# Optimization experiments

Measured on AMD Instinct MI355X. Metric: run time of the kernel, lower is better.

## Reference

```python
import jax, jax.numpy as jnp
import numpy as np

B, T, IN, H, S, OUT, NB = 64, 2048, 32, 256, 256, 32, 4
EPS = 1e-5


def setup_inputs() -> dict:
    key = jax.random.key(0)
    ks = jax.random.split(key, 13)

    def w(k, shape, fan_in):
        lim = 1.0 / np.sqrt(fan_in)
        return jax.random.uniform(k, shape, minval=-lim, maxval=lim, dtype=jnp.float32)

    return {
        "x": jax.random.normal(ks[0], (B, T, IN), dtype=jnp.float32),
        "enc_w": w(ks[1], (H, IN), IN),
        "enc_b": w(ks[2], (H,), IN),
        "wih": w(ks[3], (NB, 3 * S, H), H),    # GRU input weights per block
        "whh": w(ks[4], (NB, 3 * S, S), S),    # GRU hidden weights per block
        "b_ih": w(ks[5], (NB, 3 * S), S),      # GRU bias
        "b_n": w(ks[6], (NB, S), S),           # GRU candidate bias (bias_n)
        "g1w": w(ks[7], (NB, H, S), S),        # GLU value proj
        "g1b": w(ks[8], (NB, H), S),
        "g2w": w(ks[9], (NB, H, S), S),        # GLU gate proj
        "g2b": w(ks[10], (NB, H), S),
        "dec_w": w(ks[11], (OUT, H), H),
        "dec_b": w(ks[12], (OUT,), H),
    }


def reference(x, enc_w, enc_b, wih, whh, b_ih, b_n, g1w, g1b, g2w, g2b, dec_w, dec_b):
    # encoder: (B,T,IN) -> (B,T,H)
    h = jnp.einsum('bti,hi->bth', x, enc_w) + enc_b
    for i in range(NB):
        skip = h
        # BatchNorm (batch mode, no affine): per-channel stats over batch+time
        mean = jnp.mean(h, axis=(0, 1))
        var = jnp.mean((h - mean) ** 2, axis=(0, 1))
        hn = (h - mean) * jax.lax.rsqrt(var + EPS)
        # GRU: precompute input gates for the whole sequence
        ig = jnp.einsum('bth,gh->btg', hn, wih[i]) + b_ih[i]  # (B,T,3S)
        whh_i = whh[i]
        bn_i = b_n[i]

        def step(carry, ig_t):
            hg = carry @ whh_i.T                       # (B,3S)
            iR, iZ, iN = jnp.split(ig_t, 3, axis=-1)
            hR, hZ, hN = jnp.split(hg, 3, axis=-1)
            r = jax.nn.sigmoid(iR + hR)
            z = jax.nn.sigmoid(iZ + hZ)
            n = jnp.tanh(iN + r * (hN + bn_i))
            new = (1.0 - z) * n + z * carry
            return new, new

        h0 = jnp.zeros((x.shape[0], S), dtype=x.dtype)
        _, states = jax.lax.scan(step, h0, jnp.swapaxes(ig, 0, 1))  # (T,B,S)
        s = jax.nn.gelu(jnp.swapaxes(states, 0, 1))                 # (B,T,S)
        # GLU: w1(s) * sigmoid(w2(s)) -> (B,T,H)
        glu = (jnp.einsum('bts,hs->bth', s, g1w[i]) + g1b[i]) * \
              jax.nn.sigmoid(jnp.einsum('bts,hs->bth', s, g2w[i]) + g2b[i])
        h = skip + glu  # skip connection (dropout p=0 -> identity)
    # decoder every output_step=1 timesteps, tanh output
    out = jnp.tanh(jnp.einsum('bth,oh->bto', h, dec_w) + dec_b)
    return out
```

## Files before the change

kernel.cpp:

```cpp
#include <hip/hip_runtime.h>
#include <hip/hip_bf16.h>
#include <hip/hip_fp16.h>

constexpr int nB = 64, nT = 2048, nIN = 32, nH = 256, nS = 256, nOUT = 32, nNB = 4;
constexpr int nBT = nB * nT;

typedef __attribute__((ext_vector_type(2))) _Float16 half2v;
typedef __attribute__((ext_vector_type(4))) float f32x4;
typedef __attribute__((ext_vector_type(8))) short bf16x8;
typedef __attribute__((ext_vector_type(8))) _Float16 f16x8;
typedef __attribute__((ext_vector_type(4))) unsigned short us4;
typedef __attribute__((ext_vector_type(4))) unsigned int uint4v;

#define GLDS(gsrc, ldst)                                                        \
  __builtin_amdgcn_global_load_lds(                                             \
      (const __attribute__((address_space(1))) void*)(gsrc),                    \
      (__attribute__((address_space(3))) void*)(ldst), 16, 0, 0)

__device__ __forceinline__ float fast_exp(float x) {
  return __builtin_amdgcn_exp2f(x * 1.44269504088896f);
}
__device__ __forceinline__ float sigm(float x) {
  return __builtin_amdgcn_rcpf(1.f + fast_exp(-x));
}
__device__ __forceinline__ float tanh_f(float x) {
  float ax = fabsf(x);
  float e = fast_exp(-2.f * ax);
  float r = 1.f - 2.f * e * __builtin_amdgcn_rcpf(1.f + e);
  return copysignf(r, x);
}
__device__ __forceinline__ float gelu_f(float x) {
  float x3 = x * x * x;
  return 0.5f * x * (1.f + tanh_f(0.79788456080286536f * (x + 0.044715f * x3)));
}
__device__ __forceinline__ unsigned short f2bf(float f) {
  unsigned int u = __builtin_bit_cast(unsigned int, f);
  unsigned int r = (u + 0x7fffu + ((u >> 16) & 1u)) >> 16;
  return (unsigned short)r;
}

__global__ __launch_bounds__(256) void k_cvt_bf16(const float* __restrict__ src,
                                                  unsigned short* __restrict__ dst, int n) {
  for (int i = blockIdx.x * 256 + threadIdx.x; i < n; i += gridDim.x * 256)
    dst[i] = f2bf(src[i]);
}

__global__ __launch_bounds__(256) void k_pack_whh(const float* __restrict__ whh,
                                                  unsigned int* __restrict__ dst) {
  int idx = blockIdx.x * 256 + threadIdx.x;
  int total = nNB * 512 * 48 * 4;
  if (idx >= total) return;
  int d = idx & 3;
  int rest = idx >> 2;
  int f = rest % 48;
  int rest2 = rest / 48;
  int t = rest2 & 511;
  int i = rest2 >> 9;
  int w = t >> 6, l = t & 63;
  int jt = f / 24, fr = f % 24, g = fr / 8, s = fr % 8;
  int row = g * 256 + w * 32 + jt * 16 + (l & 15);
  int k = 32 * s + ((l >> 4) & 3) * 8 + 2 * d;
  const float* wrow = whh + ((size_t)i * 768 + row) * 256;
  unsigned short a = __builtin_bit_cast(unsigned short, (_Float16)wrow[k]);
  unsigned short b = __builtin_bit_cast(unsigned short, (_Float16)wrow[k + 1]);
  dst[idx] = (unsigned int)a | ((unsigned int)b << 16);
}

__global__ __launch_bounds__(256) void k_encoder(const float* __restrict__ x,
                                                 const float* __restrict__ ew,
                                                 const float* __restrict__ eb,
                                                 float* __restrict__ h) {
  __shared__ float xs[32][32];
  int tid = threadIdx.x;
  int r0 = blockIdx.x * 32;
  for (int q = tid; q < 32 * 32; q += 256)
    xs[q >> 5][q & 31] = x[(size_t)(r0 + (q >> 5)) * nIN + (q & 31)];
  float w[32];
#pragma unroll
  for (int k = 0; k < 32; k++) w[k] = ew[tid * 32 + k];
  float b = eb[tid];
  __syncthreads();
  for (int r = 0; r < 32; r++) {
    float acc = b;
#pragma unroll
    for (int k = 0; k < 32; k++) acc = fmaf(xs[r][k], w[k], acc);
    h[(size_t)(r0 + r) * nH + tid] = acc;
  }
}

__global__ __launch_bounds__(256) void k_bn_partial(const float* __restrict__ h,
                                                    float* __restrict__ psum,
                                                    float* __restrict__ psq) {
  int c = threadIdx.x;
  int blk = blockIdx.x;
  size_t base = (size_t)blk * 128 * nH + c;
  float s = 0.f, s2 = 0.f;
  for (int r = 0; r < 128; r++) {
    float v = h[base + (size_t)r * nH];
    s += v;
    s2 = fmaf(v, v, s2);
  }
  psum[c * 1024 + blk] = s;
  psq[c * 1024 + blk] = s2;
}

__global__ __launch_bounds__(256) void k_bn_final(const float* __restrict__ psum,
                                                  const float* __restrict__ psq,
                                                  float* __restrict__ mean,
                                                  float* __restrict__ istd) {
  int c = blockIdx.x;
  int t = threadIdx.x;
  __shared__ float rs[256], rq[256];
  float s = 0.f, q = 0.f;
#pragma unroll
  for (int p = 0; p < 4; p++) {
    s += psum[c * 1024 + t + 256 * p];
    q += psq[c * 1024 + t + 256 * p];
  }
  rs[t] = s;
  rq[t] = q;
  __syncthreads();
  for (int off = 128; off; off >>= 1) {
    if (t < off) {
      rs[t] += rs[t + off];
      rq[t] += rq[t + off];
    }
    __syncthreads();
  }
  if (t == 0) {
    float m = rs[0] * (1.f / (float)nBT);
    float v = rq[0] * (1.f / (float)nBT) - m * m;
    mean[c] = m;
    istd[c] = rsqrtf(v + 1e-5f);
  }
}

__global__ __launch_bounds__(256) void k_norm_cvt(const float* __restrict__ h,
                                                  const float* __restrict__ mean,
                                                  const float* __restrict__ istd,
                                                  unsigned short* __restrict__ hn) {
  __shared__ float ms[256], is[256];
  int t = threadIdx.x;
  ms[t] = mean[t];
  is[t] = istd[t];
  __syncthreads();
  size_t total = (size_t)nBT * (nH / 4);
  for (size_t idx = (size_t)blockIdx.x * 256 + t; idx < total; idx += (size_t)gridDim.x * 256) {
    f32x4 v = ((const f32x4*)h)[idx];
    int c0 = (int)((idx & 63) * 4);
    us4 o;
    o.x = f2bf((v.x - ms[c0 + 0]) * is[c0 + 0]);
    o.y = f2bf((v.y - ms[c0 + 1]) * is[c0 + 1]);
    o.z = f2bf((v.z - ms[c0 + 2]) * is[c0 + 2]);
    o.w = f2bf((v.w - ms[c0 + 3]) * is[c0 + 3]);
    ((us4*)hn)[idx] = o;
  }
}

__global__ __launch_bounds__(256) void k_gemm_ig(const unsigned short* __restrict__ A,
                                                 const unsigned short* __restrict__ W,
                                                 const float* __restrict__ bih,
                                                 _Float16* __restrict__ out,
                                                 int t0, int tcShift) {
  __shared__ __align__(16) unsigned short As[128 * 32];
  __shared__ __align__(16) unsigned short Bs[128 * 32];
  const int tid = threadIdx.x;
  const int lane = tid & 63, wid = tid >> 6;
  const int m0 = blockIdx.y * 128, n0 = blockIdx.x * 128;
  const int wrow = wid >> 1, wcol = wid & 1;
  const int srow = tid >> 2;
  const int scol = (tid & 3) * 8;
  const int bIdx = m0 >> tcShift;
  const int tb = (m0 & ((1 << tcShift) - 1)) + t0;
  const unsigned short* Ag = A + ((size_t)bIdx * nT + tb + srow) * 256 + scol;
  const unsigned short* Wg = W + (size_t)(n0 + srow) * 256 + scol;
  unsigned short* AsW = As + wid * 512;
  unsigned short* BsW = Bs + wid * 512;

  f32x4 acc[4][4] = {};
  for (int kt = 0; kt < 8; kt++) {
    const int ko = kt * 32;
    GLDS(Ag + ko, AsW);
    GLDS(Ag + ko + 64 * 256, AsW + 2048);
    GLDS(Wg + ko, BsW);
    GLDS(Wg + ko + 64 * 256, BsW + 2048);
    __syncthreads();
    bf16x8 af[4], bfv[4];
    const int kr = (lane >> 4) * 8;
    const int rA = wrow * 64 + (lane & 15);
    const int rB = wcol * 64 + (lane & 15);
#pragma unroll
    for (int mi = 0; mi < 4; mi++) af[mi] = *(const bf16x8*)&As[(rA + mi * 16) * 32 + kr];
#pragma unroll
    for (int ni = 0; ni < 4; ni++) bfv[ni] = *(const bf16x8*)&Bs[(rB + ni * 16) * 32 + kr];
#pragma unroll
    for (int mi = 0; mi < 4; mi++)
#pragma unroll
      for (int ni = 0; ni < 4; ni++)
        acc[mi][ni] = __builtin_amdgcn_mfma_f32_16x16x32_bf16(af[mi], bfv[ni], acc[mi][ni], 0, 0, 0);
    __syncthreads();
  }
#pragma unroll
  for (int ni = 0; ni < 4; ni++) {
    const int col = n0 + wcol * 64 + ni * 16 + (lane & 15);
    const float bv = bih[col];
#pragma unroll
    for (int mi = 0; mi < 4; mi++) {
      const int row = m0 + wrow * 64 + mi * 16 + (lane >> 4) * 4;
#pragma unroll
      for (int r = 0; r < 4; r++)
        out[(size_t)(row + r) * 768 + col] = (_Float16)(acc[mi][ni][r] + bv);
    }
  }
}

__global__ __launch_bounds__(256) void k_gemm_glu(const unsigned short* __restrict__ A,
                                                  const unsigned short* __restrict__ W1,
                                                  const unsigned short* __restrict__ W2,
                                                  const float* __restrict__ b1,
                                                  const float* __restrict__ b2,
                                                  float* __restrict__ h) {
  __shared__ __align__(16) unsigned short As[128 * 32];
  __shared__ __align__(16) unsigned short B1s[128 * 32];
  __shared__ __align__(16) unsigned short B2s[128 * 32];
  const int tid = threadIdx.x;
  const int lane = tid & 63, wid = tid >> 6;
  const int m0 = blockIdx.y * 128, n0 = blockIdx.x * 128;
  const int wrow = wid >> 1, wcol = wid & 1;
  const int srow = tid >> 2;
  const int scol = (tid & 3) * 8;
  const unsigned short* Ag = A + (size_t)(m0 + srow) * 256 + scol;
  const unsigned short* W1g = W1 + (size_t)(n0 + srow) * 256 + scol;
  const unsigned short* W2g = W2 + (size_t)(n0 + srow) * 256 + scol;
  unsigned short* AsW = As + wid * 512;
  unsigned short* B1sW = B1s + wid * 512;
  unsigned short* B2sW = B2s + wid * 512;

  f32x4 acc1[4][4] = {};
  f32x4 acc2[4][4] = {};
  for (int kt = 0; kt < 8; kt++) {
    const int ko = kt * 32;
    GLDS(Ag + ko, AsW);
    GLDS(Ag + ko + 64 * 256, AsW + 2048);
    GLDS(W1g + ko, B1sW);
    GLDS(W1g + ko + 64 * 256, B1sW + 2048);
    GLDS(W2g + ko, B2sW);
    GLDS(W2g + ko + 64 * 256, B2sW + 2048);
    __syncthreads();
    bf16x8 af[4], b1v[4], b2v[4];
    const int kr = (lane >> 4) * 8;
    const int rA = wrow * 64 + (lane & 15);
    const int rB = wcol * 64 + (lane & 15);
#pragma unroll
    for (int mi = 0; mi < 4; mi++) af[mi] = *(const bf16x8*)&As[(rA + mi * 16) * 32 + kr];
#pragma unroll
    for (int ni = 0; ni < 4; ni++) {
      b1v[ni] = *(const bf16x8*)&B1s[(rB + ni * 16) * 32 + kr];
      b2v[ni] = *(const bf16x8*)&B2s[(rB + ni * 16) * 32 + kr];
    }
#pragma unroll
    for (int mi = 0; mi < 4; mi++)
#pragma unroll
      for (int ni = 0; ni < 4; ni++) {
        acc1[mi][ni] = __builtin_amdgcn_mfma_f32_16x16x32_bf16(af[mi], b1v[ni], acc1[mi][ni], 0, 0, 0);
        acc2[mi][ni] = __builtin_amdgcn_mfma_f32_16x16x32_bf16(af[mi], b2v[ni], acc2[mi][ni], 0, 0, 0);
      }
    __syncthreads();
  }
#pragma unroll
  for (int ni = 0; ni < 4; ni++) {
    const int col = n0 + wcol * 64 + ni * 16 + (lane & 15);
    const float bv1 = b1[col];
    const float bv2 = b2[col];
#pragma unroll
    for (int mi = 0; mi < 4; mi++) {
      const int row = m0 + wrow * 64 + mi * 16 + (lane >> 4) * 4;
#pragma unroll
      for (int r = 0; r < 4; r++) {
        float v1 = acc1[mi][ni][r] + bv1;
        float v2 = acc2[mi][ni][r] + bv2;
        size_t o = (size_t)(row + r) * nH + col;
        h[o] = h[o] + v1 * sigm(v2);
      }
    }
  }
}

__global__ __launch_bounds__(512, 2) void k_gru_scan(const unsigned int* __restrict__ wpk,
                                                     const _Float16* __restrict__ ig,
                                                     const float* __restrict__ bn,
                                                     unsigned short* __restrict__ s_out,
                                                     float* __restrict__ hstate,
                                                     int Tc, int t0, int first) {
  const int tid = threadIdx.x;
  const int b = blockIdx.x;
  const int w = tid >> 6, l = tid & 63;
  const int j0 = w * 32 + (l & 15), j1 = j0 + 16;
  __shared__ __align__(16) _Float16 hlds[2][256];

  const f16x8* wb = (const f16x8*)(wpk + (size_t)tid * 192);
#define LB(i) const f16x8 B##i = wb[i];
  LB(0) LB(1) LB(2) LB(3) LB(4) LB(5) LB(6) LB(7)
  LB(8) LB(9) LB(10) LB(11) LB(12) LB(13) LB(14) LB(15)
  LB(16) LB(17) LB(18) LB(19) LB(20) LB(21) LB(22) LB(23)
  LB(24) LB(25) LB(26) LB(27) LB(28) LB(29) LB(30) LB(31)
  LB(32) LB(33) LB(34) LB(35) LB(36) LB(37) LB(38) LB(39)
  LB(40) LB(41) LB(42) LB(43) LB(44) LB(45) LB(46) LB(47)
#undef LB

  const float bn0 = bn[j0], bn1 = bn[j1];
  float h0 = first ? 0.f : hstate[b * 256 + j0];
  float h1 = first ? 0.f : hstate[b * 256 + j1];
  if (l < 16) {
    hlds[0][j0] = (_Float16)h0;
    hlds[0][j1] = (_Float16)h1;
  }
  const _Float16* igrow = ig + (size_t)b * Tc * 768;
  _Float16 cR0 = igrow[j0], cZ0 = igrow[256 + j0], cN0 = igrow[512 + j0];
  _Float16 cR1 = igrow[j1], cZ1 = igrow[256 + j1], cN1 = igrow[512 + j1];
  unsigned short* srow = s_out + ((size_t)b * nT + t0) * nS;
  __syncthreads();

  const int aoff = (l >> 4) * 8;
  int cur = 0;
  for (int t = 0; t < Tc; t++) {
    _Float16 nR0 = cR0, nZ0 = cZ0, nN0 = cN0, nR1 = cR1, nZ1 = cZ1, nN1 = cN1;
    if (t + 1 < Tc) {
      const _Float16* nx = igrow + (size_t)(t + 1) * 768;
      nR0 = nx[j0]; nZ0 = nx[256 + j0]; nN0 = nx[512 + j0];
      nR1 = nx[j1]; nZ1 = nx[256 + j1]; nN1 = nx[512 + j1];
    }
    const _Float16* hc = hlds[cur];
    const f16x8 A0 = *(const f16x8*)&hc[0 + aoff];
    const f16x8 A1 = *(const f16x8*)&hc[32 + aoff];
    const f16x8 A2 = *(const f16x8*)&hc[64 + aoff];
    const f16x8 A3 = *(const f16x8*)&hc[96 + aoff];
    const f16x8 A4 = *(const f16x8*)&hc[128 + aoff];
    const f16x8 A5 = *(const f16x8*)&hc[160 + aoff];
    const f16x8 A6 = *(const f16x8*)&hc[192 + aoff];
    const f16x8 A7 = *(const f16x8*)&hc[224 + aoff];
#define MF(a, bb, c) __builtin_amdgcn_mfma_f32_16x16x32_f16(a, bb, c, 0, 0, 0)
#define CH(acc, Ba, Bb, Bc, Bd, Be, Bf, Bg, Bh)  \
    acc = MF(A0, Ba, acc); acc = MF(A1, Bb, acc); \
    acc = MF(A2, Bc, acc); acc = MF(A3, Bd, acc); \
    acc = MF(A4, Be, acc); acc = MF(A5, Bf, acc); \
    acc = MF(A6, Bg, acc); acc = MF(A7, Bh, acc);
    f32x4 aR = {0.f, 0.f, 0.f, 0.f}, aZ = {0.f, 0.f, 0.f, 0.f}, aN = {0.f, 0.f, 0.f, 0.f};
    CH(aR, B0, B1, B2, B3, B4, B5, B6, B7)
    CH(aZ, B8, B9, B10, B11, B12, B13, B14, B15)
    CH(aN, B16, B17, B18, B19, B20, B21, B22, B23)
    float r0 = sigm((float)cR0 + aR[0]);
    float z0 = sigm((float)cZ0 + aZ[0]);
    float n0 = tanh_f((float)cN0 + r0 * (aN[0] + bn0));
    float hn0 = fmaf(z0, h0 - n0, n0);
    f32x4 bR = {0.f, 0.f, 0.f, 0.f}, bZ = {0.f, 0.f, 0.f, 0.f}, bN = {0.f, 0.f, 0.f, 0.f};
    CH(bR, B24, B25, B26, B27, B28, B29, B30, B31)
    CH(bZ, B32, B33, B34, B35, B36, B37, B38, B39)
    CH(bN, B40, B41, B42, B43, B44, B45, B46, B47)
#undef CH
#undef MF
    float r1 = sigm((float)cR1 + bR[0]);
    float z1 = sigm((float)cZ1 + bZ[0]);
    float n1 = tanh_f((float)cN1 + r1 * (bN[0] + bn1));
    float hn1 = fmaf(z1, h1 - n1, n1);
    h0 = hn0;
    h1 = hn1;
    if (l < 16) {
      hlds[cur ^ 1][j0] = (_Float16)hn0;
      hlds[cur ^ 1][j1] = (_Float16)hn1;
      srow[(size_t)t * nS + j0] = f2bf(gelu_f(hn0));
      srow[(size_t)t * nS + j1] = f2bf(gelu_f(hn1));
    }
    __syncthreads();
    cur ^= 1;
    cR0 = nR0; cZ0 = nZ0; cN0 = nN0;
    cR1 = nR1; cZ1 = nZ1; cN1 = nN1;
  }
  if (l < 16) {
    hstate[b * 256 + j0] = h0;
    hstate[b * 256 + j1] = h1;
  }
}

__global__ __launch_bounds__(256) void k_decoder(const float* __restrict__ h,
                                                 const float* __restrict__ dw,
                                                 const float* __restrict__ db,
                                                 float* __restrict__ out) {
  __shared__ float hs[8][256];
  __shared__ float ws[32][257];
  const int tid = threadIdx.x;
  for (int q = tid; q < 32 * 256; q += 256) ws[q >> 8][q & 255] = dw[q];
  const int r0 = blockIdx.x * 8;
  for (int q = tid; q < 8 * 256; q += 256)
    hs[q >> 8][q & 255] = h[(size_t)(r0 + (q >> 8)) * nH + (q & 255)];
  __syncthreads();
  const int r = tid >> 5, o = tid & 31;
  float acc = db[o];
#pragma unroll 8
  for (int k = 0; k < 256; k++) acc = fmaf(hs[r][k], ws[o][k], acc);
  out[(size_t)(r0 + r) * nOUT + o] = tanh_f(acc);
}

extern "C" void kernel_launch(void* const* d_in, const int* in_sizes, int n_in,
                              void* d_out, int out_size, void* d_ws, size_t ws_size,
                              hipStream_t stream) {
  const float* x = (const float*)d_in[0];
  const float* enc_w = (const float*)d_in[1];
  const float* enc_b = (const float*)d_in[2];
  const float* wih = (const float*)d_in[3];
  const float* whh = (const float*)d_in[4];
  const float* b_ih = (const float*)d_in[5];
  const float* b_n = (const float*)d_in[6];
  const float* g1w = (const float*)d_in[7];
  const float* g1b = (const float*)d_in[8];
  const float* g2w = (const float*)d_in[9];
  const float* g2b = (const float*)d_in[10];
  const float* dec_w = (const float*)d_in[11];
  const float* dec_b = (const float*)d_in[12];

  char* w = (char*)d_ws;
  float* h = (float*)w;                        w += (size_t)nBT * nH * 4;
  unsigned short* hs = (unsigned short*)w;     w += (size_t)nBT * nH * 2;
  float* psum = (float*)w;                     w += (size_t)256 * 1024 * 4;
  float* psq = (float*)w;                      w += (size_t)256 * 1024 * 4;
  float* mean = (float*)w;                     w += 1024;
  float* istd = (float*)w;                     w += 1024;
  float* hstate = (float*)w;                   w += (size_t)nB * nS * 4;
  unsigned short* wih_b = (unsigned short*)w;  w += (size_t)nNB * 768 * 256 * 2;
  unsigned short* g1w_b = (unsigned short*)w;  w += (size_t)nNB * 256 * 256 * 2;
  unsigned short* g2w_b = (unsigned short*)w;  w += (size_t)nNB * 256 * 256 * 2;
  unsigned int* whh_pk = (unsigned int*)w;     w += (size_t)nNB * 512 * 192 * 4;
  _Float16* ig = (_Float16*)w;
  size_t fixedBytes = (size_t)(w - (char*)d_ws);

  int tcShift = 11;
  while (tcShift > 7 && fixedBytes + (((size_t)nB << tcShift) * 768 * 2) > ws_size) tcShift--;
  const int Tc = 1 << tcShift;
  const int nChunks = nT / Tc;

  k_cvt_bf16<<<1024, 256, 0, stream>>>(wih, wih_b, nNB * 768 * 256);
  k_cvt_bf16<<<512, 256, 0, stream>>>(g1w, g1w_b, nNB * 256 * 256);
  k_cvt_bf16<<<512, 256, 0, stream>>>(g2w, g2w_b, nNB * 256 * 256);
  k_pack_whh<<<1536, 256, 0, stream>>>(whh, whh_pk);

  k_encoder<<<nBT / 32, 256, 0, stream>>>(x, enc_w, enc_b, h);

  for (int i = 0; i < nNB; i++) {
    k_bn_partial<<<1024, 256, 0, stream>>>(h, psum, psq);
    k_bn_final<<<256, 256, 0, stream>>>(psum, psq, mean, istd);
    k_norm_cvt<<<2048, 256, 0, stream>>>(h, mean, istd, hs);
    for (int c = 0; c < nChunks; c++) {
      k_gemm_ig<<<dim3(6, (nB * Tc) / 128), 256, 0, stream>>>(
          hs, wih_b + (size_t)i * 768 * 256, b_ih + i * 768, ig, c * Tc, tcShift);
      k_gru_scan<<<nB, 512, 0, stream>>>(whh_pk + (size_t)i * 512 * 192, ig, b_n + i * 256,
                                         hs, hstate, Tc, c * Tc, c == 0 ? 1 : 0);
    }
    k_gemm_glu<<<dim3(2, nBT / 128), 256, 0, stream>>>(hs, g1w_b + (size_t)i * 256 * 256,
                                                       g2w_b + (size_t)i * 256 * 256,
                                                       g1b + i * 256, g2b + i * 256, h);
  }

  k_decoder<<<nBT / 8, 256, 0, stream>>>(h, dec_w, dec_b, (float*)d_out);
}
```

Baseline: 12.27 ms.

## Spill four GRU weight fragments to LDS and interleave six MFMA chains

```diff
diff --git a/kernel.cpp b/kernel.cpp
--- a/kernel.cpp
+++ b/kernel.cpp
@@ -297,15 +297,19 @@
   const int w = tid >> 6, l = tid & 63;
   const int j0 = w * 32 + (l & 15), j1 = j0 + 16;
   __shared__ __align__(16) _Float16 hlds[2][256];
+  __shared__ __align__(16) _Float16 bfrag[4][512][8];
 
   const f16x8* wb = (const f16x8*)(wpk + (size_t)tid * 192);
+#pragma unroll
+  for (int s = 0; s < 4; s++) *(f16x8*)&bfrag[s][tid][0] = wb[44 + s];
+
 #define LB(i) const f16x8 B##i = wb[i];
   LB(0) LB(1) LB(2) LB(3) LB(4) LB(5) LB(6) LB(7)
   LB(8) LB(9) LB(10) LB(11) LB(12) LB(13) LB(14) LB(15)
   LB(16) LB(17) LB(18) LB(19) LB(20) LB(21) LB(22) LB(23)
   LB(24) LB(25) LB(26) LB(27) LB(28) LB(29) LB(30) LB(31)
   LB(32) LB(33) LB(34) LB(35) LB(36) LB(37) LB(38) LB(39)
-  LB(40) LB(41) LB(42) LB(43) LB(44) LB(45) LB(46) LB(47)
+  LB(40) LB(41) LB(42) LB(43)
 #undef LB
 
   const float bn0 = bn[j0], bn1 = bn[j1];
@@ -322,6 +326,7 @@
   __syncthreads();
 
   const int aoff = (l >> 4) * 8;
+  const char* bbase = (const char*)&bfrag[0][0][0];
   int cur = 0;
   for (int t = 0; t < Tc; t++) {
     _Float16 nR0 = cR0, nZ0 = cZ0, nN0 = cN0, nR1 = cR1, nZ1 = cZ1, nN1 = cN1;
@@ -330,35 +335,32 @@
       nR0 = nx[j0]; nZ0 = nx[256 + j0]; nN0 = nx[512 + j0];
       nR1 = nx[j1]; nZ1 = nx[256 + j1]; nN1 = nx[512 + j1];
     }
+    unsigned soff = (unsigned)tid * 16u;
+    asm volatile("" : "+v"(soff));
+    const char* bl = bbase + soff;
     const _Float16* hc = hlds[cur];
-    const f16x8 A0 = *(const f16x8*)&hc[0 + aoff];
-    const f16x8 A1 = *(const f16x8*)&hc[32 + aoff];
-    const f16x8 A2 = *(const f16x8*)&hc[64 + aoff];
-    const f16x8 A3 = *(const f16x8*)&hc[96 + aoff];
-    const f16x8 A4 = *(const f16x8*)&hc[128 + aoff];
-    const f16x8 A5 = *(const f16x8*)&hc[160 + aoff];
-    const f16x8 A6 = *(const f16x8*)&hc[192 + aoff];
-    const f16x8 A7 = *(const f16x8*)&hc[224 + aoff];
+    f32x4 aR = {0.f, 0.f, 0.f, 0.f}, aZ = {0.f, 0.f, 0.f, 0.f}, aN = {0.f, 0.f, 0.f, 0.f};
+    f32x4 bR = {0.f, 0.f, 0.f, 0.f}, bZ = {0.f, 0.f, 0.f, 0.f}, bN = {0.f, 0.f, 0.f, 0.f};
 #define MF(a, bb, c) __builtin_amdgcn_mfma_f32_16x16x32_f16(a, bb, c, 0, 0, 0)
-#define CH(acc, Ba, Bb, Bc, Bd, Be, Bf, Bg, Bh)  \
-    acc = MF(A0, Ba, acc); acc = MF(A1, Bb, acc); \
-    acc = MF(A2, Bc, acc); acc = MF(A3, Bd, acc); \
-    acc = MF(A4, Be, acc); acc = MF(A5, Bf, acc); \
-    acc = MF(A6, Bg, acc); acc = MF(A7, Bh, acc);
-    f32x4 aR = {0.f, 0.f, 0.f, 0.f}, aZ = {0.f, 0.f, 0.f, 0.f}, aN = {0.f, 0.f, 0.f, 0.f};
-    CH(aR, B0, B1, B2, B3, B4, B5, B6, B7)
-    CH(aZ, B8, B9, B10, B11, B12, B13, B14, B15)
-    CH(aN, B16, B17, B18, B19, B20, B21, B22, B23)
+#define SREG(s, R0v, Z0v, N0v, R1v, Z1v, N1v) {            \
+    const f16x8 As = *(const f16x8*)&hc[(s) * 32 + aoff];  \
+    aR = MF(As, R0v, aR); aZ = MF(As, Z0v, aZ);            \
+    aN = MF(As, N0v, aN); bR = MF(As, R1v, bR);            \
+    bZ = MF(As, Z1v, bZ); bN = MF(As, N1v, bN); }
+    SREG(0, B0, B8, B16, B24, B32, B40)
+    SREG(1, B1, B9, B17, B25, B33, B41)
+    SREG(2, B2, B10, B18, B26, B34, B42)
+    SREG(3, B3, B11, B19, B27, B35, B43)
+    SREG(4, B4, B12, B20, B28, B36, (*(const f16x8*)(bl + 0 * 8192)))
+    SREG(5, B5, B13, B21, B29, B37, (*(const f16x8*)(bl + 1 * 8192)))
+    SREG(6, B6, B14, B22, B30, B38, (*(const f16x8*)(bl + 2 * 8192)))
+    SREG(7, B7, B15, B23, B31, B39, (*(const f16x8*)(bl + 3 * 8192)))
+#undef SREG
+#undef MF
     float r0 = sigm((float)cR0 + aR[0]);
     float z0 = sigm((float)cZ0 + aZ[0]);
     float n0 = tanh_f((float)cN0 + r0 * (aN[0] + bn0));
     float hn0 = fmaf(z0, h0 - n0, n0);
-    f32x4 bR = {0.f, 0.f, 0.f, 0.f}, bZ = {0.f, 0.f, 0.f, 0.f}, bN = {0.f, 0.f, 0.f, 0.f};
-    CH(bR, B24, B25, B26, B27, B28, B29, B30, B31)
-    CH(bZ, B32, B33, B34, B35, B36, B37, B38, B39)
-    CH(bN, B40, B41, B42, B43, B44, B45, B46, B47)
-#undef CH
-#undef MF
     float r1 = sigm((float)cR1 + bR[0]);
     float z1 = sigm((float)cZ1 + bZ[0]);
     float n1 = tanh_f((float)cN1 + r1 * (bN[0] + bn1));
```

Measured after the change: 12.52 ms. 2.1% more time.
